# Kernel optimization log

Measured on AMD Instinct MI355X. Metric: run time of the kernel, lower is better.

Reference implementation:

```python
import jax, jax.numpy as jnp
import numpy as np

B, S, D, H = 2, 2048, 1024, 16

def setup_inputs() -> dict:
    key = jax.random.key(0)
    k_x, k_wq, k_bq, k_wk, k_wv = jax.random.split(key, 5)
    return {
        "x": jax.random.normal(k_x, (B, S, D), dtype=jnp.float32),
        "Wq": jax.random.normal(k_wq, (D, D), dtype=jnp.float32) / 100.0,
        "Bq": jax.random.normal(k_bq, (1, D), dtype=jnp.float32) / 100.0,
        "Wk": jax.random.normal(k_wk, (D, D), dtype=jnp.float32) / 100.0,
        "Wv": jax.random.normal(k_wv, (D, D), dtype=jnp.float32) / 100.0,
        "n_heads": H,
    }

def reference(x, Wq, Bq, Wk, Wv, n_heads):
    b, s, d = x.shape
    dh = d // n_heads
    # Projections
    Q = x @ Wq + Bq          # [b, s, d]
    K = x @ Wk               # [b, s, d]
    V = x @ Wv               # [b, s, d]
    # Unconventional head split: last dim -> (d_head, n_heads), heads LAST
    Q = Q.reshape(b, s, dh, n_heads)
    K = K.reshape(b, s, dh, n_heads)
    V = V.reshape(b, s, dh, n_heads)
    # NOTE: original scales by sqrt(d_model), not sqrt(d_head)
    scale = 1.0 / np.sqrt(d).astype(np.float32)
    scores = jnp.einsum('bidh,bjdh->bijh', Q, K) * scale  # [b, i, j, h]
    attn = jax.nn.softmax(scores, axis=2)                 # softmax over j
    out = jnp.einsum('bijh,bjdh->bidh', attn, V)          # [b, i, dh, h]
    return out.reshape(b, s, d)                            # merge_heads
```

## Files before the change

### kernel.cpp

```cpp
#include <hip/hip_runtime.h>

#define B_ 2
#define S_ 2048
#define D_ 1024
#define H_ 16

typedef __attribute__((ext_vector_type(8))) short short8;
typedef __attribute__((ext_vector_type(8))) unsigned short ushort8;
typedef __attribute__((ext_vector_type(4))) short short4v;
typedef __attribute__((ext_vector_type(4))) float f32x4;

__device__ __forceinline__ unsigned short f2b(float f){
  unsigned u = __float_as_uint(f);
  u += 0x7fffu + ((u >> 16) & 1u);
  return (unsigned short)(u >> 16);
}
__device__ __forceinline__ float b2f(unsigned short b){
  return __uint_as_float(((unsigned)b) << 16);
}
__device__ __forceinline__ float fast_exp2(float x){
#if __has_builtin(__builtin_amdgcn_exp2f)
  return __builtin_amdgcn_exp2f(x);
#else
  return exp2f(x);
#endif
}
__device__ __forceinline__ unsigned pack_trunc(unsigned u_lo, unsigned u_hi){
#if __has_builtin(__builtin_amdgcn_perm)
  return __builtin_amdgcn_perm(u_hi, u_lo, 0x07060302u);
#else
  return (u_lo >> 16) | (u_hi & 0xffff0000u);
#endif
}
__device__ __forceinline__ f32x4 mfma16(short8 a, short8 b, f32x4 c){
  return __builtin_amdgcn_mfma_f32_16x16x32_bf16(a, b, c, 0, 0, 0);
}
__device__ __forceinline__ f32x4 mfma16k16(short4v a, short4v b, f32x4 c){
#if __has_builtin(__builtin_amdgcn_mfma_f32_16x16x16bf16_1k)
  return __builtin_amdgcn_mfma_f32_16x16x16bf16_1k(a, b, c, 0, 0, 0);
#else
  asm("v_mfma_f32_16x16x16_bf16 %0, %1, %2, %0" : "+v"(c) : "v"(a), "v"(b));
  return c;
#endif
}
__device__ __forceinline__ void gload_lds16(const void* g, void* l){
  __builtin_amdgcn_global_load_lds((const __attribute__((address_space(1))) unsigned int*)g,
                                   (__attribute__((address_space(3))) unsigned int*)l, 16, 0, 0);
}

__global__ __launch_bounds__(256) void prep(const float* __restrict__ x,
                                            const float* __restrict__ Wq,
                                            const float* __restrict__ Wk,
                                            const float* __restrict__ Wv,
                                            unsigned short* __restrict__ xbf,
                                            unsigned short* __restrict__ wT){
  const int z = blockIdx.z;
  if (z == 3){
    int lb = blockIdx.y * 32 + blockIdx.x;
    int i = (lb * 256 + threadIdx.x) * 16;
    #pragma unroll
    for (int half = 0; half < 2; half++){
      f32x4 a = *(const f32x4*)(x + i + half * 8);
      f32x4 b = *(const f32x4*)(x + i + half * 8 + 4);
      ushort8 o;
      o[0]=f2b(a[0]); o[1]=f2b(a[1]); o[2]=f2b(a[2]); o[3]=f2b(a[3]);
      o[4]=f2b(b[0]); o[5]=f2b(b[1]); o[6]=f2b(b[2]); o[7]=f2b(b[3]);
      *(ushort8*)(xbf + i + half * 8) = o;
    }
    return;
  }
  const float* W = (z == 0) ? Wq : ((z == 1) ? Wk : Wv);
  __shared__ float tile[32][33];
  int nb = blockIdx.x * 32, kb = blockIdx.y * 32;
  int tx = threadIdx.x & 31, ty = threadIdx.x >> 5;
  #pragma unroll
  for (int it = 0; it < 4; it++){
    int row = ty + it * 8;
    tile[row][tx] = W[(size_t)(kb + row) * D_ + nb + tx];
  }
  __syncthreads();
  unsigned short* outp = wT + (size_t)z * D_ * D_;
  #pragma unroll
  for (int it = 0; it < 4; it++){
    int row = ty + it * 8;
    int n = nb + row;
    int np = ((n & 15) << 6) | (n >> 4);
    outp[(size_t)np * D_ + kb + tx] = f2b(tile[tx][row]);
  }
}

__global__ __launch_bounds__(256) void qkv_gemm(const unsigned short* __restrict__ xbf,
                                                const unsigned short* __restrict__ wT,
                                                const float* __restrict__ Bq,
                                                unsigned short* __restrict__ qatt,
                                                unsigned short* __restrict__ katt,
                                                unsigned short* __restrict__ vatt){
  __shared__ char SM[34816];
  unsigned short* Ct = (unsigned short*)SM;
  const int proj = blockIdx.z;
  const int mbase = blockIdx.y * 128, nbase = blockIdx.x * 128;
  const unsigned short* bsrc = wT + (size_t)proj * D_ * D_;
  const int t = threadIdx.x, w = t >> 6, lane = t & 63, ln = lane & 15, hi = lane >> 4;
  const int wr = w >> 1, wc = w & 1;
  const int srow = t >> 2, scol = (t & 3) << 3;
  f32x4 acc[4][4] = {};

  #pragma unroll
  for (int i = 0; i < 2; i++){
    gload_lds16(xbf  + (size_t)(mbase + srow + i * 64) * D_ + scol, SM + w * 1024 + i * 4096);
    gload_lds16(bsrc + (size_t)(nbase + srow + i * 64) * D_ + scol, SM + 8192 + w * 1024 + i * 4096);
  }
  __syncthreads();

  int cur = 0;
  for (int ks = 0; ks < D_; ks += 32){
    if (ks + 32 < D_){
      char* nb_ = SM + (cur ^ 1) * 16384;
      #pragma unroll
      for (int i = 0; i < 2; i++){
        gload_lds16(xbf  + (size_t)(mbase + srow + i * 64) * D_ + ks + 32 + scol, nb_ + w * 1024 + i * 4096);
        gload_lds16(bsrc + (size_t)(nbase + srow + i * 64) * D_ + ks + 32 + scol, nb_ + 8192 + w * 1024 + i * 4096);
      }
    }
    const unsigned short* At = (const unsigned short*)(SM + cur * 16384);
    const unsigned short* Bt = (const unsigned short*)(SM + cur * 16384 + 8192);
    short8 af[4], bf[4];
    #pragma unroll
    for (int q = 0; q < 4; q++) af[q] = *(const short8*)&At[(wr * 64 + q * 16 + ln) * 32 + hi * 8];
    #pragma unroll
    for (int p = 0; p < 4; p++) bf[p] = *(const short8*)&Bt[(wc * 64 + p * 16 + ln) * 32 + hi * 8];
    #pragma unroll
    for (int q = 0; q < 4; q++)
      #pragma unroll
      for (int p = 0; p < 4; p++)
        acc[q][p] = mfma16(af[q], bf[p], acc[q][p]);
    __syncthreads();
    cur ^= 1;
  }

  const float qscale = 0.04508422002778011f;
  const int b = mbase >> 11, ms = mbase & 2047;

  if (proj == 2){
    #pragma unroll
    for (int p = 0; p < 4; p++)
      #pragma unroll
      for (int q = 0; q < 4; q++)
        #pragma unroll
        for (int r = 0; r < 4; r++)
          Ct[(wc*64 + p*16 + ln) * 136 + wr*64 + q*16 + hi*4 + r] = f2b(acc[q][p][r]);
    __syncthreads();
    #pragma unroll
    for (int j = 0; j < 8; j++){
      int u = j * 256 + t;
      int col = u >> 4, s0 = (u & 15) * 8;
      int h = blockIdx.x * 2 + (col >> 6), r = col & 63;
      short8 v = *(const short8*)&Ct[col * 136 + s0];
      *(short8*)&vatt[((size_t)(b*16 + h) * 64 + r) * 2048 + ms + s0] = v;
    }
  } else {
    const int hglob = blockIdx.x * 2 + wc;
    #pragma unroll
    for (int p = 0; p < 4; p++){
      float bqv = (proj == 0) ? Bq[(p*16 + ln)*16 + hglob] : 0.f;
      #pragma unroll
      for (int q = 0; q < 4; q++)
        #pragma unroll
        for (int r = 0; r < 4; r++){
          float v = acc[q][p][r];
          if (proj == 0) v = (v + bqv) * qscale;
          Ct[(wr*64 + q*16 + hi*4 + r) * 136 + wc*64 + p*16 + ln] = f2b(v);
        }
    }
    __syncthreads();
    unsigned short* dstb = (proj == 0) ? qatt : katt;
    #pragma unroll
    for (int j = 0; j < 8; j++){
      int u = j * 256 + t;
      int hl = u >> 10, rem = u & 1023, sl = rem >> 3, r0 = (rem & 7) * 8;
      int h = blockIdx.x * 2 + hl;
      short8 v = *(const short8*)&Ct[sl * 136 + hl*64 + r0];
      *(short8*)&dstb[((size_t)(b*16 + h) * 2048 + ms + sl) * 64 + r0] = v;
    }
  }
}

template<int NS>
__global__ __launch_bounds__(256) void attn_fwd(const unsigned short* __restrict__ qatt,
                                                const unsigned short* __restrict__ katt,
                                                const unsigned short* __restrict__ vatt,
                                                unsigned short* __restrict__ pnum,
                                                float* __restrict__ pden){
  __shared__ unsigned short Kt[2][64 * 64];
  __shared__ unsigned short Vt[2][64 * 64];
  const int t = threadIdx.x, w = t >> 6, lane = t & 63, ln = lane & 15, hi = lane >> 4;
  const int bid = blockIdx.x;
  const int bpx = (512 * NS) / 8;
  const int L = (bid & 7) * bpx + (bid >> 3);
  const int bh = L / (16 * NS);
  const int rem = L % (16 * NS);
  const int z = rem >> 4, qc = rem & 15;
  const int b = bh >> 4, h = bh & 15;
  const int q0 = qc * 128 + w * 32;
  const int kvbase = z * (S_ / NS);
  const int NT = (S_ / NS) / 64;
  const unsigned short* Qh = qatt + (size_t)bh * S_ * 64;
  const unsigned short* Kh = katt + (size_t)bh * S_ * 64;
  const unsigned short* Vh = vatt + (size_t)bh * 64 * S_;

  short8 qf[2][2];
  #pragma unroll
  for (int qb = 0; qb < 2; qb++)
    #pragma unroll
    for (int kc = 0; kc < 2; kc++)
      qf[qb][kc] = *(const short8*)&Qh[(size_t)(q0 + qb * 16 + ln) * 64 + kc * 32 + hi * 8];

  const int srow = w * 16 + (lane >> 3);
  const int scol0 = ((lane & 7) * 16) ^ ((srow & 7) << 4);
  const int scol1 = ((lane & 7) * 16) ^ (((srow + 8) & 7) << 4);

  f32x4 acc[2][4] = {};
  f32x4 accd[2] = {};
  const short4v vones = {(short)0x3F80, (short)0x3F80, (short)0x3F80, (short)0x3F80};

  {
    int kv = kvbase;
    gload_lds16(Kh + (size_t)(kv + srow) * 64 + (scol0 >> 1),     (char*)&Kt[0][0] + w * 2048);
    gload_lds16(Kh + (size_t)(kv + srow + 8) * 64 + (scol1 >> 1), (char*)&Kt[0][0] + w * 2048 + 1024);
    gload_lds16(Vh + (size_t)srow * S_ + kv + (scol0 >> 1),       (char*)&Vt[0][0] + w * 2048);
    gload_lds16(Vh + (size_t)(srow + 8) * S_ + kv + (scol1 >> 1), (char*)&Vt[0][0] + w * 2048 + 1024);
  }
  __syncthreads();

  int cur = 0;
  for (int tt = 0; tt < NT; ++tt){
    if (tt + 1 < NT){
      int kv = kvbase + (tt + 1) * 64;
      int nb = cur ^ 1;
      gload_lds16(Kh + (size_t)(kv + srow) * 64 + (scol0 >> 1),     (char*)&Kt[nb][0] + w * 2048);
      gload_lds16(Kh + (size_t)(kv + srow + 8) * 64 + (scol1 >> 1), (char*)&Kt[nb][0] + w * 2048 + 1024);
      gload_lds16(Vh + (size_t)srow * S_ + kv + (scol0 >> 1),       (char*)&Vt[nb][0] + w * 2048);
      gload_lds16(Vh + (size_t)(srow + 8) * S_ + kv + (scol1 >> 1), (char*)&Vt[nb][0] + w * 2048 + 1024);
    }
    const unsigned short* Kc = &Kt[cur][0];
    const unsigned short* Vc = &Vt[cur][0];

    short8 kf[4][2];
    #pragma unroll
    for (int kb = 0; kb < 4; kb++)
      #pragma unroll
      for (int kc = 0; kc < 2; kc++){
        int eb = (((kc * 64 + hi * 16) ^ ((ln & 7) << 4)) >> 1);
        kf[kb][kc] = *(const short8*)&Kc[(kb * 16 + ln) * 64 + eb];
      }

    short4v pa[2][4];
    #pragma unroll
    for (int qb = 0; qb < 2; qb++)
      #pragma unroll
      for (int kb = 0; kb < 4; kb++){
        f32x4 zz = {0.f, 0.f, 0.f, 0.f};
        zz = mfma16(kf[kb][0], qf[qb][0], zz);
        zz = mfma16(kf[kb][1], qf[qb][1], zz);
        unsigned u0 = __float_as_uint(fast_exp2(zz[0]));
        unsigned u1 = __float_as_uint(fast_exp2(zz[1]));
        unsigned u2 = __float_as_uint(fast_exp2(zz[2]));
        unsigned u3 = __float_as_uint(fast_exp2(zz[3]));
        union { unsigned u[2]; short4v s; } pk;
        pk.u[0] = pack_trunc(u0, u1);
        pk.u[1] = pack_trunc(u2, u3);
        pa[qb][kb] = pk.s;
      }

    #pragma unroll
    for (int kb = 0; kb < 4; kb++){
      accd[0] = mfma16k16(pa[0][kb], vones, accd[0]);
      accd[1] = mfma16k16(pa[1][kb], vones, accd[1]);
    }

    #pragma unroll
    for (int cb = 0; cb < 4; cb++)
      #pragma unroll
      for (int kb = 0; kb < 4; kb++){
        int eb = (((kb * 32 + hi * 8) ^ ((ln & 7) << 4)) >> 1);
        short4v vf = *(const short4v*)&Vc[(cb * 16 + ln) * 64 + eb];
        acc[0][cb] = mfma16k16(pa[0][kb], vf, acc[0][cb]);
        acc[1][cb] = mfma16k16(pa[1][kb], vf, acc[1][cb]);
      }
    __syncthreads();
    cur ^= 1;
  }

  if (ln == 0){
    #pragma unroll
    for (int qb = 0; qb < 2; qb++)
      #pragma unroll
      for (int r = 0; r < 4; r++)
        pden[((size_t)(z * 2 + b) * S_ + q0 + qb * 16 + hi * 4 + r) * 16 + h] = accd[qb][r];
  }

  const size_t rowb = (size_t)(z * 2 + b) * S_;
  #pragma unroll
  for (int qb = 0; qb < 2; qb++)
    #pragma unroll
    for (int cb = 0; cb < 4; cb++)
      #pragma unroll
      for (int r = 0; r < 4; r++){
        int qrow = q0 + qb * 16 + hi * 4 + r;
        pnum[(rowb + qrow) * 1024 + h * 64 + cb * 16 + ln] = f2b(acc[qb][cb][r]);
      }
}

template<int NSPLIT>
__global__ __launch_bounds__(256) void attn_reduce(const unsigned short* __restrict__ pnum,
                                                   const float* __restrict__ pden,
                                                   float* __restrict__ out){
  __shared__ float L[4 * 1056];
  const int t = threadIdx.x;
  const int row_l = t >> 6, lane = t & 63;
  const int grow = blockIdx.x * 4 + row_l;
  const int e0 = lane * 16;
  const int h = e0 >> 6;
  float den = 0.f;
  float nsum[16];
  #pragma unroll
  for (int j = 0; j < 16; j++) nsum[j] = 0.f;
  #pragma unroll
  for (int z = 0; z < NSPLIT; z++){
    const size_t prow = (size_t)z * 4096 + grow;
    den += pden[prow * 16 + h];
    #pragma unroll
    for (int c = 0; c < 2; c++){
      ushort8 nv = *(const ushort8*)&pnum[prow * 1024 + e0 + c * 8];
      #pragma unroll
      for (int k = 0; k < 8; k++) nsum[c*8 + k] += b2f(nv[k]);
    }
  }
  float rinv = 1.0f / den;
  #pragma unroll
  for (int j = 0; j < 16; j++){
    int col = e0 + j;
    L[row_l * 1056 + col + (col >> 5)] = nsum[j] * rinv;
  }
  __syncthreads();
  const int d0 = lane * 16;
  #pragma unroll
  for (int c = 0; c < 4; c++){
    f32x4 o;
    #pragma unroll
    for (int k = 0; k < 4; k++){
      int d = d0 + c * 4 + k;
      int e = ((d & 15) << 6) | (d >> 4);
      o[k] = L[row_l * 1056 + e + (e >> 5)];
    }
    *(f32x4*)&out[(size_t)grow * 1024 + d0 + c * 4] = o;
  }
}

extern "C" void kernel_launch(void* const* d_in, const int* in_sizes, int n_in,
                              void* d_out, int out_size, void* d_ws, size_t ws_size,
                              hipStream_t stream){
  const float* x  = (const float*)d_in[0];
  const float* Wq = (const float*)d_in[1];
  const float* Bq = (const float*)d_in[2];
  const float* Wk = (const float*)d_in[3];
  const float* Wv = (const float*)d_in[4];
  char* ws = (char*)d_ws;
  const size_t MB = 1024 * 1024;
  unsigned short* qatt = (unsigned short*)(ws);
  unsigned short* katt = (unsigned short*)(ws + 8 * MB);
  unsigned short* vatt = (unsigned short*)(ws + 16 * MB);
  unsigned short* xbf  = (unsigned short*)(ws + 24 * MB);
  unsigned short* wT   = (unsigned short*)(ws + 32 * MB);
  float* outp = (float*)d_out;

  prep<<<dim3(32, 32, 4), 256, 0, stream>>>(x, Wq, Wk, Wv, xbf, wT);
  qkv_gemm<<<dim3(8, 32, 3), 256, 0, stream>>>(xbf, wT, Bq, qatt, katt, vatt);

  if (ws_size >= 59 * MB){
    const int NS = 4;
    unsigned short* pnum = (unsigned short*)(ws + 24 * MB);
    float* pden = (float*)(ws + 24 * MB + (size_t)NS * 8 * MB);
    attn_fwd<NS><<<512 * NS, 256, 0, stream>>>(qatt, katt, vatt, pnum, pden);
    attn_reduce<NS><<<1024, 256, 0, stream>>>(pnum, pden, outp);
  } else if (ws_size >= 42 * MB){
    const int NS = 2;
    unsigned short* pnum = (unsigned short*)(ws + 24 * MB);
    float* pden = (float*)(ws + 24 * MB + (size_t)NS * 8 * MB);
    attn_fwd<NS><<<512 * NS, 256, 0, stream>>>(qatt, katt, vatt, pnum, pden);
    attn_reduce<NS><<<1024, 256, 0, stream>>>(pnum, pden, outp);
  } else {
    const int NS = 1;
    unsigned short* pnum = (unsigned short*)(ws + 24 * MB);
    float* pden = (float*)(ws + 24 * MB + (size_t)NS * 8 * MB);
    attn_fwd<NS><<<512 * NS, 256, 0, stream>>>(qatt, katt, vatt, pnum, pden);
    attn_reduce<NS><<<1024, 256, 0, stream>>>(pnum, pden, outp);
  }
}
```

Baseline: 102.4 us.

## Replace double-buffered K/V LDS tiles with single buffer and wave priority boost

Removes double-buffering of the K/V tiles in the attention kernel. Each iteration now loads its tile into a single LDS buffer, synchronizes, computes, then synchronizes again. s_setprio raises wave priority during the MFMA section. This halves LDS use per block so more blocks can be resident, relying on inter-block overlap in place of intra-block prefetch. The cost is that each block stalls on every tile load.

```diff
diff --git a/kernel.cpp b/kernel.cpp
--- a/kernel.cpp
+++ b/kernel.cpp
@@ -191,8 +191,8 @@
                                                 const unsigned short* __restrict__ vatt,
                                                 unsigned short* __restrict__ pnum,
                                                 float* __restrict__ pden){
-  __shared__ unsigned short Kt[2][64 * 64];
-  __shared__ unsigned short Vt[2][64 * 64];
+  __shared__ unsigned short Kt[64 * 64];
+  __shared__ unsigned short Vt[64 * 64];
   const int t = threadIdx.x, w = t >> 6, lane = t & 63, ln = lane & 15, hi = lane >> 4;
   const int bid = blockIdx.x;
   const int bpx = (512 * NS) / 8;
@@ -223,35 +223,22 @@
   f32x4 accd[2] = {};
   const short4v vones = {(short)0x3F80, (short)0x3F80, (short)0x3F80, (short)0x3F80};
 
-  {
-    int kv = kvbase;
-    gload_lds16(Kh + (size_t)(kv + srow) * 64 + (scol0 >> 1),     (char*)&Kt[0][0] + w * 2048);
-    gload_lds16(Kh + (size_t)(kv + srow + 8) * 64 + (scol1 >> 1), (char*)&Kt[0][0] + w * 2048 + 1024);
-    gload_lds16(Vh + (size_t)srow * S_ + kv + (scol0 >> 1),       (char*)&Vt[0][0] + w * 2048);
-    gload_lds16(Vh + (size_t)(srow + 8) * S_ + kv + (scol1 >> 1), (char*)&Vt[0][0] + w * 2048 + 1024);
-  }
-  __syncthreads();
-
-  int cur = 0;
   for (int tt = 0; tt < NT; ++tt){
-    if (tt + 1 < NT){
-      int kv = kvbase + (tt + 1) * 64;
-      int nb = cur ^ 1;
-      gload_lds16(Kh + (size_t)(kv + srow) * 64 + (scol0 >> 1),     (char*)&Kt[nb][0] + w * 2048);
-      gload_lds16(Kh + (size_t)(kv + srow + 8) * 64 + (scol1 >> 1), (char*)&Kt[nb][0] + w * 2048 + 1024);
-      gload_lds16(Vh + (size_t)srow * S_ + kv + (scol0 >> 1),       (char*)&Vt[nb][0] + w * 2048);
-      gload_lds16(Vh + (size_t)(srow + 8) * S_ + kv + (scol1 >> 1), (char*)&Vt[nb][0] + w * 2048 + 1024);
-    }
-    const unsigned short* Kc = &Kt[cur][0];
-    const unsigned short* Vc = &Vt[cur][0];
-
+    const int kv = kvbase + tt * 64;
+    gload_lds16(Kh + (size_t)(kv + srow) * 64 + (scol0 >> 1),     (char*)Kt + w * 2048);
+    gload_lds16(Kh + (size_t)(kv + srow + 8) * 64 + (scol1 >> 1), (char*)Kt + w * 2048 + 1024);
+    gload_lds16(Vh + (size_t)srow * S_ + kv + (scol0 >> 1),       (char*)Vt + w * 2048);
+    gload_lds16(Vh + (size_t)(srow + 8) * S_ + kv + (scol1 >> 1), (char*)Vt + w * 2048 + 1024);
+    __syncthreads();
+
+    __builtin_amdgcn_s_setprio(1);
     short8 kf[4][2];
     #pragma unroll
     for (int kb = 0; kb < 4; kb++)
       #pragma unroll
       for (int kc = 0; kc < 2; kc++){
         int eb = (((kc * 64 + hi * 16) ^ ((ln & 7) << 4)) >> 1);
-        kf[kb][kc] = *(const short8*)&Kc[(kb * 16 + ln) * 64 + eb];
+        kf[kb][kc] = *(const short8*)&Kt[(kb * 16 + ln) * 64 + eb];
       }
 
     short4v pa[2][4];
@@ -283,12 +270,12 @@
       #pragma unroll
       for (int kb = 0; kb < 4; kb++){
         int eb = (((kb * 32 + hi * 8) ^ ((ln & 7) << 4)) >> 1);
-        short4v vf = *(const short4v*)&Vc[(cb * 16 + ln) * 64 + eb];
+        short4v vf = *(const short4v*)&Vt[(cb * 16 + ln) * 64 + eb];
         acc[0][cb] = mfma16k16(pa[0][kb], vf, acc[0][cb]);
         acc[1][cb] = mfma16k16(pa[1][kb], vf, acc[1][cb]);
       }
-    __syncthreads();
-    cur ^= 1;
+    __builtin_amdgcn_s_setprio(0);
+    __syncthreads();
   }
 
   if (ln == 0){
```

Result: no change. 103.3 us (+0.9%).

## Use 16x16x32 bf16 MFMA for PV by permuting K rows to match layout

Applied to the files above, without the earlier changes.

Replaces the 16x16x16 bf16 MFMAs in the P·V and denominator accumulation with 16x16x32 MFMAs. Two score tiles are packed into one 8-element operand. K rows are loaded into LDS in a permuted order so the packed P fragment lines up with contiguous V columns. This halves the number of MFMA instructions and V LDS reads per tile. It relies on the row permutation being exactly consistent with the accumulator output layout.

```diff
diff --git a/kernel.cpp b/kernel.cpp
--- a/kernel.cpp
+++ b/kernel.cpp
@@ -34,14 +34,6 @@
 }
 __device__ __forceinline__ f32x4 mfma16(short8 a, short8 b, f32x4 c){
   return __builtin_amdgcn_mfma_f32_16x16x32_bf16(a, b, c, 0, 0, 0);
-}
-__device__ __forceinline__ f32x4 mfma16k16(short4v a, short4v b, f32x4 c){
-#if __has_builtin(__builtin_amdgcn_mfma_f32_16x16x16bf16_1k)
-  return __builtin_amdgcn_mfma_f32_16x16x16bf16_1k(a, b, c, 0, 0, 0);
-#else
-  asm("v_mfma_f32_16x16x16_bf16 %0, %1, %2, %0" : "+v"(c) : "v"(a), "v"(b));
-  return c;
-#endif
 }
 __device__ __forceinline__ void gload_lds16(const void* g, void* l){
   __builtin_amdgcn_global_load_lds((const __attribute__((address_space(1))) unsigned int*)g,
@@ -218,15 +210,19 @@
   const int srow = w * 16 + (lane >> 3);
   const int scol0 = ((lane & 7) * 16) ^ ((srow & 7) << 4);
   const int scol1 = ((lane & 7) * 16) ^ (((srow + 8) & 7) << 4);
+  const int t0 = srow, t1 = srow + 8;
+  const int kp0 = ((t0 >> 5) << 5) | (((t0 >> 2) & 3) << 3) | (((t0 >> 4) & 1) << 2) | (t0 & 3);
+  const int kp1 = ((t1 >> 5) << 5) | (((t1 >> 2) & 3) << 3) | (((t1 >> 4) & 1) << 2) | (t1 & 3);
 
   f32x4 acc[2][4] = {};
   f32x4 accd[2] = {};
-  const short4v vones = {(short)0x3F80, (short)0x3F80, (short)0x3F80, (short)0x3F80};
+  const short8 vones8 = {(short)0x3F80, (short)0x3F80, (short)0x3F80, (short)0x3F80,
+                         (short)0x3F80, (short)0x3F80, (short)0x3F80, (short)0x3F80};
 
   {
     int kv = kvbase;
-    gload_lds16(Kh + (size_t)(kv + srow) * 64 + (scol0 >> 1),     (char*)&Kt[0][0] + w * 2048);
-    gload_lds16(Kh + (size_t)(kv + srow + 8) * 64 + (scol1 >> 1), (char*)&Kt[0][0] + w * 2048 + 1024);
+    gload_lds16(Kh + (size_t)(kv + kp0) * 64 + (scol0 >> 1), (char*)&Kt[0][0] + w * 2048);
+    gload_lds16(Kh + (size_t)(kv + kp1) * 64 + (scol1 >> 1), (char*)&Kt[0][0] + w * 2048 + 1024);
     gload_lds16(Vh + (size_t)srow * S_ + kv + (scol0 >> 1),       (char*)&Vt[0][0] + w * 2048);
     gload_lds16(Vh + (size_t)(srow + 8) * S_ + kv + (scol1 >> 1), (char*)&Vt[0][0] + w * 2048 + 1024);
   }
@@ -237,8 +233,8 @@
     if (tt + 1 < NT){
       int kv = kvbase + (tt + 1) * 64;
       int nb = cur ^ 1;
-      gload_lds16(Kh + (size_t)(kv + srow) * 64 + (scol0 >> 1),     (char*)&Kt[nb][0] + w * 2048);
-      gload_lds16(Kh + (size_t)(kv + srow + 8) * 64 + (scol1 >> 1), (char*)&Kt[nb][0] + w * 2048 + 1024);
+      gload_lds16(Kh + (size_t)(kv + kp0) * 64 + (scol0 >> 1), (char*)&Kt[nb][0] + w * 2048);
+      gload_lds16(Kh + (size_t)(kv + kp1) * 64 + (scol1 >> 1), (char*)&Kt[nb][0] + w * 2048 + 1024);
       gload_lds16(Vh + (size_t)srow * S_ + kv + (scol0 >> 1),       (char*)&Vt[nb][0] + w * 2048);
       gload_lds16(Vh + (size_t)(srow + 8) * S_ + kv + (scol1 >> 1), (char*)&Vt[nb][0] + w * 2048 + 1024);
     }
@@ -254,38 +250,42 @@
         kf[kb][kc] = *(const short8*)&Kc[(kb * 16 + ln) * 64 + eb];
       }
 
-    short4v pa[2][4];
+    short8 pa8[2][2];
     #pragma unroll
     for (int qb = 0; qb < 2; qb++)
       #pragma unroll
-      for (int kb = 0; kb < 4; kb++){
-        f32x4 zz = {0.f, 0.f, 0.f, 0.f};
-        zz = mfma16(kf[kb][0], qf[qb][0], zz);
-        zz = mfma16(kf[kb][1], qf[qb][1], zz);
-        unsigned u0 = __float_as_uint(fast_exp2(zz[0]));
-        unsigned u1 = __float_as_uint(fast_exp2(zz[1]));
-        unsigned u2 = __float_as_uint(fast_exp2(zz[2]));
-        unsigned u3 = __float_as_uint(fast_exp2(zz[3]));
-        union { unsigned u[2]; short4v s; } pk;
-        pk.u[0] = pack_trunc(u0, u1);
-        pk.u[1] = pack_trunc(u2, u3);
-        pa[qb][kb] = pk.s;
-      }
-
-    #pragma unroll
-    for (int kb = 0; kb < 4; kb++){
-      accd[0] = mfma16k16(pa[0][kb], vones, accd[0]);
-      accd[1] = mfma16k16(pa[1][kb], vones, accd[1]);
-    }
+      for (int W = 0; W < 2; W++){
+        f32x4 za = {0.f, 0.f, 0.f, 0.f};
+        za = mfma16(kf[2*W][0], qf[qb][0], za);
+        za = mfma16(kf[2*W][1], qf[qb][1], za);
+        f32x4 zb = {0.f, 0.f, 0.f, 0.f};
+        zb = mfma16(kf[2*W+1][0], qf[qb][0], zb);
+        zb = mfma16(kf[2*W+1][1], qf[qb][1], zb);
+        unsigned a0 = __float_as_uint(fast_exp2(za[0]));
+        unsigned a1 = __float_as_uint(fast_exp2(za[1]));
+        unsigned a2 = __float_as_uint(fast_exp2(za[2]));
+        unsigned a3 = __float_as_uint(fast_exp2(za[3]));
+        unsigned b0 = __float_as_uint(fast_exp2(zb[0]));
+        unsigned b1 = __float_as_uint(fast_exp2(zb[1]));
+        unsigned b2 = __float_as_uint(fast_exp2(zb[2]));
+        unsigned b3 = __float_as_uint(fast_exp2(zb[3]));
+        union { unsigned u[4]; short8 s; } pk;
+        pk.u[0] = pack_trunc(a0, a1);
+        pk.u[1] = pack_trunc(a2, a3);
+        pk.u[2] = pack_trunc(b0, b1);
+        pk.u[3] = pack_trunc(b2, b3);
+        pa8[qb][W] = pk.s;
+        accd[qb] = mfma16(pa8[qb][W], vones8, accd[qb]);
+      }
 
     #pragma unroll
     for (int cb = 0; cb < 4; cb++)
       #pragma unroll
-      for (int kb = 0; kb < 4; kb++){
-        int eb = (((kb * 32 + hi * 8) ^ ((ln & 7) << 4)) >> 1);
-        short4v vf = *(const short4v*)&Vc[(cb * 16 + ln) * 64 + eb];
-        acc[0][cb] = mfma16k16(pa[0][kb], vf, acc[0][cb]);
-        acc[1][cb] = mfma16k16(pa[1][kb], vf, acc[1][cb]);
+      for (int W = 0; W < 2; W++){
+        int eb = (((W * 64 + hi * 16) ^ ((ln & 7) << 4)) >> 1);
+        short8 vf = *(const short8*)&Vc[(cb * 16 + ln) * 64 + eb];
+        acc[0][cb] = mfma16(pa8[0][W], vf, acc[0][cb]);
+        acc[1][cb] = mfma16(pa8[1][W], vf, acc[1][cb]);
       }
     __syncthreads();
     cur ^= 1;
```

After: 100.00 us. 1.02x faster.
